# Kernel optimization log

Measured on AMD Instinct MI355X. Metric: run time of the kernel, lower is better.

Reference implementation:

```python
import jax, jax.numpy as jnp
import numpy as np

N = 65536        # total nodes
E = 2097152      # total edges (avg degree 32)
B = 1024         # graphs / proteins
FXD = 78         # atom feature dim
DIM = 32         # GIN hidden dim
EMB = 128        # protein embedding dim
OUTD = 128       # output_dim
VOCAB = 26       # CHARPROTLEN + 1
PLEN = 1000      # protein sequence length (conv in_channels)
KS = 8           # conv kernel size
CLEN = EMB - KS + 1  # 121
NF = 32          # n_filters


def setup_inputs() -> dict:
    key = jax.random.key(0)
    ks = jax.random.split(key, 30)
    g = lambda k, s: (jax.random.normal(k, s, dtype=jnp.float32) * 0.05)
    inp = {
        "x": jax.random.normal(ks[0], (N, FXD), dtype=jnp.float32),
        "edge_index": jax.random.randint(ks[1], (2, E), 0, N, dtype=jnp.int32),
        "batch": jnp.sort(jax.random.randint(ks[2], (N,), 0, B, dtype=jnp.int32)),
        "target": jax.random.randint(ks[3], (B, PLEN), 0, VOCAB, dtype=jnp.int32),
        # GIN layer 1 MLP
        "w1a": g(ks[4], (FXD, DIM)), "b1a": jnp.zeros((DIM,), jnp.float32),
        "w1b": g(ks[5], (DIM, DIM)), "b1b": jnp.zeros((DIM,), jnp.float32),
        # GIN layers 2-5 MLPs (stacked)
        "wa": g(ks[6], (4, DIM, DIM)), "ba": jnp.zeros((4, DIM), jnp.float32),
        "wb": g(ks[7], (4, DIM, DIM)), "bb": jnp.zeros((4, DIM), jnp.float32),
        # BatchNorm affine params for bn1..bn5
        "gamma": jnp.ones((5, DIM), jnp.float32),
        "beta": jnp.zeros((5, DIM), jnp.float32),
        # drug head
        "w_fcxd": g(ks[8], (DIM, OUTD)), "b_fcxd": jnp.zeros((OUTD,), jnp.float32),
        # protein branch
        "emb": g(ks[9], (VOCAB, EMB)),
        "conv_w": g(ks[10], (NF, PLEN, KS)),  # OIH layout
        "conv_b": jnp.zeros((NF,), jnp.float32),
        "w_fcxt": g(ks[11], (NF * CLEN, OUTD)), "b_fcxt": jnp.zeros((OUTD,), jnp.float32),
        # joint head
        "w_fc1": g(ks[12], (256, 1024)), "b_fc1": jnp.zeros((1024,), jnp.float32),
        "w_fc2": g(ks[13], (1024, 256)), "b_fc2": jnp.zeros((256,), jnp.float32),
        "w_out": g(ks[14], (256, 1)), "b_out": jnp.zeros((1,), jnp.float32),
    }
    return inp


def reference(x, edge_index, batch, target,
              w1a, b1a, w1b, b1b, wa, ba, wb, bb, gamma, beta,
              w_fcxd, b_fcxd, emb, conv_w, conv_b, w_fcxt, b_fcxt,
              w_fc1, b_fc1, w_fc2, b_fc2, w_out, b_out):
    n_nodes = x.shape[0]
    n_graphs = target.shape[0]
    src, dst = edge_index[0], edge_index[1]

    def gin_bn(h, wi, bi, wo, bo, g, bt):
        # GINConv (eps=0): nn((1+eps)*x + sum_{j->i} x_j), then ReLU, then BatchNorm1d (batch stats)
        agg = jax.ops.segment_sum(h[src], dst, num_segments=n_nodes) + h
        h = jnp.maximum(agg @ wi + bi, 0.0) @ wo + bo
        h = jnp.maximum(h, 0.0)
        m = h.mean(axis=0)
        v = h.var(axis=0)  # biased, matches torch BN normalization
        return g * (h - m) * jax.lax.rsqrt(v + 1e-5) + bt

    h = gin_bn(x, w1a, b1a, w1b, b1b, gamma[0], beta[0])
    for i in range(4):
        h = gin_bn(h, wa[i], ba[i], wb[i], bb[i], gamma[i + 1], beta[i + 1])

    # global add pool over graphs
    hg = jax.ops.segment_sum(h, batch, num_segments=n_graphs)  # [B, 32]
    xd = jnp.maximum(hg @ w_fcxd + b_fcxd, 0.0)  # [B, 128] (dropout inactive in eval)

    # protein branch: embed then Conv1d over the embedding axis (in_channels = seq positions)
    e = emb[target]  # [B, 1000, 128]
    c = jax.lax.conv_general_dilated(e, conv_w, window_strides=(1,), padding="VALID",
                                     dimension_numbers=("NCH", "OIH", "NCH"))
    c = c + conv_b[None, :, None]  # [B, 32, 121]
    xt = c.reshape(n_graphs, NF * CLEN) @ w_fcxt + b_fcxt  # [B, 128], no activation in original

    xc = jnp.concatenate([xd, xt], axis=1)  # [B, 256]
    xc = jnp.maximum(xc @ w_fc1 + b_fc1, 0.0)
    xc = jnp.maximum(xc @ w_fc2 + b_fc2, 0.0)
    return xc @ w_out + b_out  # [B, 1]
```

## Files before the change

### kernel.cpp

```cpp
#include <hip/hip_runtime.h>
#include <hip/hip_fp16.h>

#define N_NODES 65536
#define N_EDGES 2097152
#define NB      1024
#define FXD     78
#define DIM     32
#define EMBD    128
#define OUTD    128
#define VOCAB   26
#define PLEN    1000
#define KS      8
#define CLEN    121
#define NF      32
#define FCX     (NF*CLEN)
#define NBKT    256
#define EPB     8192
#define NSLICE  256
#define EROW2   156
#define ECHUNK  13


__global__ __launch_bounds__(256) void k_bhist(
    const int* __restrict__ ei, int* __restrict__ bktCnt)
{
    __shared__ int h[NBKT];
    int tid = threadIdx.x;
    h[tid] = 0;
    __syncthreads();
    long base = (long)blockIdx.x * EPB;
    #pragma unroll 4
    for (int q=0; q<EPB/256; ++q) {
        int d = ei[N_EDGES + base + q*256 + tid];
        atomicAdd(&h[d>>8], 1);
    }
    __syncthreads();
    atomicAdd(&bktCnt[tid], h[tid]);
}

__global__ __launch_bounds__(256) void k_bscan(
    const int* __restrict__ bktCnt, int* __restrict__ bktBase, int* __restrict__ bktCur)
{
    __shared__ int s[NBKT];
    int t = threadIdx.x;
    int v = bktCnt[t];
    s[t] = v;
    __syncthreads();
    for (int off=1; off<256; off<<=1) {
        int tv = (t >= off) ? s[t-off] : 0;
        __syncthreads();
        s[t] += tv;
        __syncthreads();
    }
    int ex = s[t] - v;
    bktBase[t] = ex;
    bktCur[t] = ex;
    if (t == 255) bktBase[256] = s[255];
}

__global__ __launch_bounds__(256) void k_bucketA(
    const int* __restrict__ ei, int* __restrict__ bktCur, unsigned int* __restrict__ pairs)
{
    __shared__ unsigned int raw[EPB];
    __shared__ unsigned int srt[EPB];
    __shared__ unsigned char bOf[EPB];
    __shared__ int hist[NBKT], sc[NBKT], lcur[NBKT], gbase[NBKT];
    int tid = threadIdx.x;
    hist[tid] = 0;
    __syncthreads();
    int eb = blockIdx.x * EPB;
    for (int i=tid; i<EPB; i+=256) {
        int s = ei[eb+i];
        int d = ei[N_EDGES+eb+i];
        raw[i] = ((unsigned int)d<<16) | (unsigned int)s;
        atomicAdd(&hist[d>>8], 1);
    }
    __syncthreads();
    int v = hist[tid];
    sc[tid] = v;
    __syncthreads();
    for (int off=1; off<256; off<<=1) {
        int tv = (tid >= off) ? sc[tid-off] : 0;
        __syncthreads();
        sc[tid] += tv;
        __syncthreads();
    }
    int ex = sc[tid] - v;
    sc[tid] = ex;
    lcur[tid] = ex;
    gbase[tid] = atomicAdd(&bktCur[tid], v);
    __syncthreads();
    for (int i=tid; i<EPB; i+=256) {
        unsigned int p = raw[i];
        int k = p >> 24;
        int pos = atomicAdd(&lcur[k], 1);
        srt[pos] = p;
        bOf[pos] = (unsigned char)k;
    }
    __syncthreads();
    for (int i=tid; i<EPB; i+=256) {
        int k = bOf[i];
        pairs[gbase[k] + (i - sc[k])] = srt[i];
    }
}

__global__ __launch_bounds__(256) void k_fillB(
    const int* __restrict__ bktBase, const unsigned int* __restrict__ pairs,
    int* __restrict__ rowptr, int* __restrict__ csr)
{
    __shared__ int hist[256], sc[256], cur[256];
    int b = blockIdx.x, tid = threadIdx.x;
    int node0 = b*256;
    hist[tid] = 0;
    __syncthreads();
    int s = bktBase[b], e = bktBase[b+1];
    for (int i = s + tid; i < e; i += 256)
        atomicAdd(&hist[(pairs[i] >> 16) & 255], 1);
    __syncthreads();
    int v = hist[tid];
    sc[tid] = v;
    __syncthreads();
    for (int off=1; off<256; off<<=1) {
        int tv = (tid >= off) ? sc[tid-off] : 0;
        __syncthreads();
        sc[tid] += tv;
        __syncthreads();
    }
    int base = s + sc[tid] - v;
    rowptr[node0 + tid] = base;
    cur[tid] = base;
    if (b == NBKT-1 && tid == 255) rowptr[N_NODES] = N_EDGES;
    __syncthreads();
    for (int i = s + tid; i < e; i += 256) {
        unsigned int p = pairs[i];
        int pos = atomicAdd(&cur[(p >> 16) & 255], 1);
        csr[pos] = (int)(p & 0xFFFFu);
    }
}


__global__ __launch_bounds__(256) void k_l1_transform(
    const float* __restrict__ x, const float* __restrict__ w,
    __half* __restrict__ t)
{
    __shared__ float wS[FXD*DIM];
    for (int i = threadIdx.x; i < FXD*DIM; i += 256) wS[i] = w[i];
    __syncthreads();
    int node = blockIdx.x*256 + threadIdx.x;
    float acc[DIM];
    #pragma unroll
    for (int d=0; d<DIM; ++d) acc[d] = 0.f;
    const float* xr = x + (long)node*FXD;
    for (int j=0; j<FXD; ++j) {
        float xv = xr[j];
        #pragma unroll
        for (int d=0; d<DIM; ++d) acc[d] += xv * wS[j*DIM+d];
    }
    union { __half2 h2[16]; uint4 u4[4]; } pk;
    #pragma unroll
    for (int q=0; q<16; ++q) pk.h2[q] = __floats2half2_rn(acc[2*q], acc[2*q+1]);
    uint4* dst4 = (uint4*)(t + (long)node*DIM);
    #pragma unroll
    for (int q=0; q<4; ++q) dst4[q] = pk.u4[q];
}

__global__ __launch_bounds__(256) void k_transform(
    const float* __restrict__ z, const float* __restrict__ part,
    const float* __restrict__ gamma, const float* __restrict__ beta, int layer,
    const float* __restrict__ w, __half* __restrict__ t)
{
    __shared__ float wS[DIM*DIM];
    __shared__ float red[4][64];
    __shared__ float sS[2*DIM];
    int tid = threadIdx.x;
    for (int i=tid; i<DIM*DIM; i+=256) wS[i] = w[i];
    {
        int ch = tid & 63, qq = tid >> 6;
        float s = 0.f;
        for (int i = qq*64; i < qq*64 + 64; ++i) s += part[(i<<6) + ch];
        red[qq][ch] = s;
    }
    __syncthreads();
    if (tid < DIM) {
        float tots = red[0][tid]+red[1][tid]+red[2][tid]+red[3][tid];
        float totq = red[0][DIM+tid]+red[1][DIM+tid]+red[2][DIM+tid]+red[3][DIM+tid];
        float mean = tots * (1.f/N_NODES);
        float var  = totq * (1.f/N_NODES) - mean*mean;
        float sc = gamma[layer*DIM+tid] * rsqrtf(var + 1e-5f);
        sS[tid] = sc;
        sS[DIM+tid] = beta[layer*DIM+tid] - mean*sc;
    }
    __syncthreads();
    int node = blockIdx.x*256 + tid;
    float h[DIM];
    const float4* z4 = (const float4*)(z + (long)node*DIM);
    #pragma unroll
    for (int q=0; q<DIM/4; ++q) {
        float4 v = z4[q];
        h[q*4+0]=v.x; h[q*4+1]=v.y; h[q*4+2]=v.z; h[q*4+3]=v.w;
    }
    #pragma unroll
    for (int d=0; d<DIM; ++d) h[d] = h[d]*sS[d] + sS[DIM+d];
    float acc[DIM];
    #pragma unroll
    for (int d=0; d<DIM; ++d) acc[d] = 0.f;
    #pragma unroll
    for (int j=0; j<DIM; ++j) {
        float hv = h[j];
        #pragma unroll
        for (int d=0; d<DIM; ++d) acc[d] += hv * wS[j*DIM+d];
    }
    union { __half2 h2[16]; uint4 u4[4]; } pk;
    #pragma unroll
    for (int q=0; q<16; ++q) pk.h2[q] = __floats2half2_rn(acc[2*q], acc[2*q+1]);
    uint4* dst4 = (uint4*)(t + (long)node*DIM);
    #pragma unroll
    for (int q=0; q<4; ++q) dst4[q] = pk.u4[q];
}

__global__ __launch_bounds__(256) void k_gather_mlp(
    const int* __restrict__ rowptr, const int* __restrict__ csr,
    const __half* __restrict__ t,
    const float* __restrict__ bi, const float* __restrict__ wo, const float* __restrict__ bo,
    float* __restrict__ z, float* __restrict__ part)
{
    __shared__ float wS[DIM*DIM];
    __shared__ float bS[2*DIM];
    __shared__ float stS[2*DIM];
    int tid = threadIdx.x;
    for (int i=tid; i<DIM*DIM; i+=256) wS[i]=wo[i];
    if (tid<DIM) bS[tid]=bi[tid];
    else if (tid<2*DIM) bS[tid]=bo[tid-DIM];
    if (tid<2*DIM) stS[tid]=0.f;
    __syncthreads();
    int g = tid >> 3;
    int l = tid & 7;
    int node = blockIdx.x*32 + g;
    const uint2* t4 = (const uint2*)t;
    uint2 sv = t4[(long)node*8 + l];
    float2 p0 = __half22float2(*(const __half2*)&sv.x);
    float2 p1 = __half22float2(*(const __half2*)&sv.y);
    float a0=p0.x, a1=p0.y, a2=p1.x, a3=p1.y;
    float c0=0.f, c1=0.f, c2=0.f, c3=0.f;
    int s0 = rowptr[node], s1 = rowptr[node+1];
    int e = s0;
    for (; e+8 <= s1; e+=8) {
        int myIdx = csr[e + l];
        #pragma unroll
        for (int k=0; k<8; ++k) {
            int idx = __shfl(myIdx, k, 8);
            uint2 v = t4[(long)idx*8 + l];
            float2 q0 = __half22float2(*(const __half2*)&v.x);
            float2 q1 = __half22float2(*(const __half2*)&v.y);
            if (k & 1) { c0+=q0.x; c1+=q0.y; c2+=q1.x; c3+=q1.y; }
            else       { a0+=q0.x; a1+=q0.y; a2+=q1.x; a3+=q1.y; }
        }
    }
    if (e+4 <= s1) {
        int myIdx = csr[e + (l & 3)];
        #pragma unroll
        for (int k=0; k<4; ++k) {
            int idx = __shfl(myIdx, k, 8);
            uint2 v = t4[(long)idx*8 + l];
            float2 q0 = __half22float2(*(const __half2*)&v.x);
            float2 q1 = __half22float2(*(const __half2*)&v.y);
            if (k & 1) { c0+=q0.x; c1+=q0.y; c2+=q1.x; c3+=q1.y; }
            else       { a0+=q0.x; a1+=q0.y; a2+=q1.x; a3+=q1.y; }
        }
        e += 4;
    }
    for (; e<s1; ++e) {
        uint2 v = t4[(long)csr[e]*8 + l];
        float2 q0 = __half22float2(*(const __half2*)&v.x);
        float2 q1 = __half22float2(*(const __half2*)&v.y);
        a0+=q0.x; a1+=q0.y; a2+=q1.x; a3+=q1.y;
    }
    float ua[4];
    ua[0] = fmaxf(a0+c0 + bS[4*l+0], 0.f);
    ua[1] = fmaxf(a1+c1 + bS[4*l+1], 0.f);
    ua[2] = fmaxf(a2+c2 + bS[4*l+2], 0.f);
    ua[3] = fmaxf(a3+c3 + bS[4*l+3], 0.f);
    float zz[4];
    #pragma unroll
    for (int q=0; q<4; ++q) zz[q] = bS[DIM + 4*l + q];
    const float4* w4 = (const float4*)wS;
    #pragma unroll
    for (int j=0; j<DIM; ++j) {
        float uj = __shfl(ua[j & 3], j >> 2, 8);
        float4 wv = w4[j*8 + l];
        zz[0]+=uj*wv.x; zz[1]+=uj*wv.y; zz[2]+=uj*wv.z; zz[3]+=uj*wv.w;
    }
    #pragma unroll
    for (int q=0; q<4; ++q) zz[q] = fmaxf(zz[q], 0.f);
    ((float4*)z)[(long)node*8 + l] = make_float4(zz[0], zz[1], zz[2], zz[3]);
    float sr[4], qr[4];
    #pragma unroll
    for (int q=0; q<4; ++q) { sr[q] = zz[q]; qr[q] = zz[q]*zz[q]; }
    #pragma unroll
    for (int q=0; q<4; ++q) {
        sr[q] += __shfl_down(sr[q], 32, 64); qr[q] += __shfl_down(qr[q], 32, 64);
        sr[q] += __shfl_down(sr[q], 16, 64); qr[q] += __shfl_down(qr[q], 16, 64);
        sr[q] += __shfl_down(sr[q],  8, 64); qr[q] += __shfl_down(qr[q],  8, 64);
    }
    if ((tid & 63) < 8) {
        #pragma unroll
        for (int q=0; q<4; ++q) {
            atomicAdd(&stS[4*l+q],       sr[q]);
            atomicAdd(&stS[DIM+4*l+q],   qr[q]);
        }
    }
    __syncthreads();
    if (tid < 2*DIM)
        atomicAdd(&part[((blockIdx.x & (NSLICE-1))<<6) + tid], stS[tid]);
}

__global__ __launch_bounds__(256) void k_scaleshift(
    const float* __restrict__ part,
    const float* __restrict__ gamma, const float* __restrict__ beta,
    int layer, float* __restrict__ ss)
{
    __shared__ float red[4][64];
    __shared__ float totS[64];
    int t = threadIdx.x;
    int ch = t & 63, q = t >> 6;
    float s = 0.f;
    for (int i = q*64; i < q*64 + 64; ++i) s += part[(i<<6) + ch];
    red[q][ch] = s;
    __syncthreads();
    if (t < 64) totS[t] = red[0][t]+red[1][t]+red[2][t]+red[3][t];
    __syncthreads();
    if (t < DIM) {
        float mean = totS[t] * (1.f/N_NODES);
        float var  = totS[DIM+t] * (1.f/N_NODES) - mean*mean;
        float sc = gamma[layer*DIM+t] * rsqrtf(var + 1e-5f);
        ss[t] = sc;
        ss[DIM+t] = beta[layer*DIM+t] - mean*sc;
    }
}

__global__ __launch_bounds__(256) void k_pool(
    const float* __restrict__ z, const float* __restrict__ ss,
    const int* __restrict__ batch, float* __restrict__ hg)
{
    int tid = threadIdx.x;
    int node = blockIdx.x*32 + (tid>>3);
    int cq = tid & 7;
    float4 v = ((const float4*)z)[(long)node*8 + cq];
    float4 sc = ((const float4*)ss)[cq];
    float4 sh = ((const float4*)ss)[8 + cq];
    v.x = v.x*sc.x + sh.x; v.y = v.y*sc.y + sh.y;
    v.z = v.z*sc.z + sh.z; v.w = v.w*sc.w + sh.w;
    int b = batch[node];
    int b0 = __shfl(b, 0, 64);
    int b7 = __shfl(b, 63, 64);
    if (b0 == b7) {
        #pragma unroll
        for (int off=8; off<64; off<<=1) {
            v.x += __shfl_xor(v.x, off, 64);
            v.y += __shfl_xor(v.y, off, 64);
            v.z += __shfl_xor(v.z, off, 64);
            v.w += __shfl_xor(v.w, off, 64);
        }
        if ((tid & 63) < 8) {
            float* dst = hg + (long)b0*DIM + cq*4;
            atomicAdd(dst+0, v.x); atomicAdd(dst+1, v.y);
            atomicAdd(dst+2, v.z); atomicAdd(dst+3, v.w);
        }
    } else {
        float* dst = hg + (long)b*DIM + cq*4;
        atomicAdd(dst+0, v.x); atomicAdd(dst+1, v.y);
        atomicAdd(dst+2, v.z); atomicAdd(dst+3, v.w);
    }
}

__global__ __launch_bounds__(128) void k_xd(
    const float* __restrict__ hg, const float* __restrict__ w,
    const float* __restrict__ bias, float* __restrict__ xc)
{
    int b = blockIdx.x, n = threadIdx.x;
    __shared__ float hS[DIM];
    if (n < DIM) hS[n] = hg[b*DIM+n];
    __syncthreads();
    float acc = bias[n];
    #pragma unroll
    for (int r=0; r<DIM; ++r) acc += hS[r]*w[r*OUTD+n];
    xc[b*256 + n] = fmaxf(acc, 0.f);
}


__global__ __launch_bounds__(256) void k_cw_transpose(
    const float* __restrict__ cw, __half* __restrict__ cwT)
{
    int g = blockIdx.x*256 + threadIdx.x;
    int i = g >> 8;
    int j = g & 255;
    int o = j >> 3, k = j & 7;
    cwT[g] = __float2half(cw[o*(PLEN*KS) + i*KS + k]);
}

__global__ __launch_bounds__(256) void k_convA(
    const int* __restrict__ target, const __half* __restrict__ cwTh,
    __half* __restrict__ G)
{
    __shared__ int sortedS[PLEN];
    __shared__ int meta[3*VOCAB+2];
    int* cntS = meta;
    int* segS = meta + VOCAB;
    int* curS = meta + 2*VOCAB + 1;
    int bb = blockIdx.x, j = threadIdx.x;
    int b = bb >> 1, sub = bb & 1;
    if (j < VOCAB) cntS[j] = 0;
    __syncthreads();
    int tloc[4];
    #pragma unroll
    for (int q=0; q<4; ++q) {
        int i = j + q*256;
        if (i < PLEN) {
            tloc[q] = target[b*PLEN+i];
            atomicAdd(&cntS[tloc[q]], 1);
        } else tloc[q] = -1;
    }
    __syncthreads();
    if (j == 0) {
        int run = 0;
        for (int v=0; v<VOCAB; ++v) { segS[v]=run; run += cntS[v]; }
        segS[VOCAB] = run;
    }
    __syncthreads();
    if (j < VOCAB) curS[j] = segS[j];
    __syncthreads();
    #pragma unroll
    for (int q=0; q<4; ++q) {
        int i = j + q*256;
        if (i < PLEN) {
            int pos = atomicAdd(&curS[tloc[q]], 1);
            sortedS[pos] = i;
        }
    }
    __syncthreads();
    int w = j >> 6;
    int lane = j & 63;
    int half32 = lane >> 5;
    int c32 = lane & 31;
    const uint4* cw4 = (const uint4*)cwTh;
    __half2 hz = __float2half2_rn(0.f);
    int v0 = 13*sub, v1 = v0 + 13;
    int segbase = segS[v0];
    int tot = segS[v1] - segbase;
    for (int v=v0; v<v1; ++v) {
        int s = segS[v], e2 = segS[v+1];
        int wv = (tot > 0) ? ((s - segbase)*4)/tot : 0;
        if (wv > 3) wv = 3;
        if (wv != w) continue;
        float facc[8];
        #pragma unroll
        for (int q=0; q<8; ++q) facc[q] = 0.f;
        int p = s;
        for (; p+16 <= e2; p += 16) {
            __half2 h0=hz, h1=hz, h2=hz, h3=hz;
            #pragma unroll
            for (int u=0; u<8; ++u) {
                int i0 = sortedS[p+2*u], i1 = sortedS[p+2*u+1];
                int row = half32 ? i1 : i0;
                uint4 q4 = cw4[row*32 + c32];
                const __half2* hh = (const __half2*)&q4;
                h0 = __hadd2(h0, hh[0]); h1 = __hadd2(h1, hh[1]);
                h2 = __hadd2(h2, hh[2]); h3 = __hadd2(h3, hh[3]);
            }
            float2 f0=__half22float2(h0), f1=__half22float2(h1),
                   f2=__half22float2(h2), f3=__half22float2(h3);
            facc[0]+=f0.x; facc[1]+=f0.y; facc[2]+=f1.x; facc[3]+=f1.y;
            facc[4]+=f2.x; facc[5]+=f2.y; facc[6]+=f3.x; facc[7]+=f3.y;
        }
        for (; p+2 <= e2; p += 2) {
            int i0 = sortedS[p], i1 = sortedS[p+1];
            int row = half32 ? i1 : i0;
            uint4 q4 = cw4[row*32 + c32];
            const __half2* hh = (const __half2*)&q4;
            float2 f0=__half22float2(hh[0]), f1=__half22float2(hh[1]),
                   f2=__half22float2(hh[2]), f3=__half22float2(hh[3]);
            facc[0]+=f0.x; facc[1]+=f0.y; facc[2]+=f1.x; facc[3]+=f1.y;
            facc[4]+=f2.x; facc[5]+=f2.y; facc[6]+=f3.x; facc[7]+=f3.y;
        }
        if (p < e2 && half32 == 0) {
            uint4 q4 = cw4[sortedS[p]*32 + c32];
            const __half2* hh = (const __half2*)&q4;
            float2 f0=__half22float2(hh[0]), f1=__half22float2(hh[1]),
                   f2=__half22float2(hh[2]), f3=__half22float2(hh[3]);
            facc[0]+=f0.x; facc[1]+=f0.y; facc[2]+=f1.x; facc[3]+=f1.y;
            facc[4]+=f2.x; facc[5]+=f2.y; facc[6]+=f3.x; facc[7]+=f3.y;
        }
        #pragma unroll
        for (int q=0; q<8; ++q) facc[q] += __shfl_xor(facc[q], 32, 64);
        if (half32 == 0) {
            __half2 o0 = __floats2half2_rn(facc[0], facc[1]);
            __half2 o1 = __floats2half2_rn(facc[2], facc[3]);
            __half2 o2 = __floats2half2_rn(facc[4], facc[5]);
            __half2 o3 = __floats2half2_rn(facc[6], facc[7]);
            uint4 pk;
            pk.x = *(unsigned int*)&o0; pk.y = *(unsigned int*)&o1;
            pk.z = *(unsigned int*)&o2; pk.w = *(unsigned int*)&o3;
            ((uint4*)(G + ((long)b*VOCAB + v)*256))[c32] = pk;
        }
    }
}

__global__ __launch_bounds__(256) void k_convB(
    const float* __restrict__ emb, const __half* __restrict__ G,
    const float* __restrict__ conv_b, float* __restrict__ c)
{
    __shared__ __align__(16) char buf[21632];
    __shared__ float cbS[NF];
    __half* GsH = (__half*)buf;
    float*  U   = (float*)(buf + 13312);
    float*  stage = (float*)buf;
    int b = blockIdx.x, j = threadIdx.x;
    if (j < NF) cbS[j] = conv_b[j];
    {
        const uint4* gsrc = (const uint4*)(G + (long)b*VOCAB*256);
        uint4* gdst = (uint4*)GsH;
        for (int i=j; i<832; i+=256) gdst[i] = gsrc[i];
    }
    int o = j >> 3, pg = j & 7;
    int t0 = pg*16;
    int tcnt = (t0+16 <= CLEN) ? 16 : (CLEN - t0);
    float out[16];
    __syncthreads();
    #pragma unroll
    for (int q=0; q<16; ++q) out[q] = cbS[o];
    for (int ch=0; ch<2; ++ch) {
        __syncthreads();
        for (int i=j; i<ECHUNK*EMBD; i+=256) {
            int v = i >> 7, tt = i & 127;
            U[v*EROW2 + tt + 4*(tt>>4)] = emb[(ch*ECHUNK + v)*EMBD + tt];
        }
        __syncthreads();
        for (int vv=0; vv<ECHUNK; ++vv) {
            uint4 gv = *(const uint4*)(GsH + (ch*ECHUNK+vv)*256 + o*8);
            const __half2* gh = (const __half2*)&gv;
            float2 ga = __half22float2(gh[0]), gb = __half22float2(gh[1]);
            float2 gc = __half22float2(gh[2]), gd = __half22float2(gh[3]);
            float g[8] = {ga.x,ga.y,gb.x,gb.y,gc.x,gc.y,gd.x,gd.y};
            const float* ev = &U[vv*EROW2 + 20*pg];
            float4 E0 = *(const float4*)(ev);
            float4 E1 = *(const float4*)(ev+4);
            float4 E2 = *(const float4*)(ev+8);
            float4 E3 = *(const float4*)(ev+12);
            float4 E4 = *(const float4*)(ev+20);
            float4 E5 = *(const float4*)(ev+24);
            float e[24] = {E0.x,E0.y,E0.z,E0.w, E1.x,E1.y,E1.z,E1.w,
                           E2.x,E2.y,E2.z,E2.w, E3.x,E3.y,E3.z,E3.w,
                           E4.x,E4.y,E4.z,E4.w, E5.x,E5.y,E5.z,E5.w};
            #pragma unroll
            for (int q=0; q<16; ++q) {
                float s = 0.f;
                #pragma unroll
                for (int k=0; k<KS; ++k) s += e[q+k]*g[k];
                out[q] += s;
            }
        }
    }
    __syncthreads();
    for (int q=0; q<tcnt; ++q) stage[o*CLEN + t0 + q] = out[q];
    __syncthreads();
    for (int idx=j; idx<FCX; idx+=256)
        c[(long)b*FCX + idx] = stage[idx];
}

#define XT_GB  16
#define XT_NS  16
#define XT_KS  (FCX/XT_NS)
#define XT_BK  22
#define XT_NCH (XT_KS/XT_BK)
__global__ __launch_bounds__(256) void k_xt(
    const float* __restrict__ c, const float* __restrict__ w,
    float* __restrict__ xtp)
{
    __shared__ float cS[XT_GB][XT_BK];
    __shared__ float wS[XT_BK][128];
    int b0 = blockIdx.x * XT_GB;
    int ks0 = blockIdx.y * XT_KS;
    int tid = threadIdx.x;
    int g2 = tid >> 5;
    int co = tid & 31;
    int cg0 = tid / XT_BK, ck0 = tid - cg0*XT_BK;
    int i1 = tid + 256;
    int cg1 = i1 / XT_BK, ck1 = i1 - cg1*XT_BK;
    float wreg[11], creg0, creg1;
    {
        int k0 = ks0;
        #pragma unroll
        for (int q=0; q<11; ++q) {
            int idx = tid + q*256;
            wreg[q] = w[(long)(k0 + (idx>>7))*OUTD + (idx & 127)];
        }
        creg0 = c[(long)(b0+cg0)*FCX + k0 + ck0];
        if (tid < 96) creg1 = c[(long)(b0+cg1)*FCX + k0 + ck1];
    }
    float acc[2][4];
    #pragma unroll
    for (int q=0; q<2; ++q)
      #pragma unroll
      for (int p=0; p<4; ++p) acc[q][p] = 0.f;
    for (int ch=0; ch<XT_NCH; ++ch) {
        #pragma unroll
        for (int q=0; q<11; ++q) {
            int idx = tid + q*256;
            wS[idx>>7][idx & 127] = wreg[q];
        }
        cS[cg0][ck0] = creg0;
        if (tid < 96) cS[cg1][ck1] = creg1;
        __syncthreads();
        if (ch+1 < XT_NCH) {
            int k0 = ks0 + (ch+1)*XT_BK;
            #pragma unroll
            for (int q=0; q<11; ++q) {
                int idx = tid + q*256;
                wreg[q] = w[(long)(k0 + (idx>>7))*OUTD + (idx & 127)];
            }
            creg0 = c[(long)(b0+cg0)*FCX + k0 + ck0];
            if (tid < 96) creg1 = c[(long)(b0+cg1)*FCX + k0 + ck1];
        }
        #pragma unroll
        for (int k2=0; k2<XT_BK/2; ++k2) {
            float2 cv0 = *(const float2*)&cS[2*g2  ][2*k2];
            float2 cv1 = *(const float2*)&cS[2*g2+1][2*k2];
            float4 wv0 = *(const float4*)&wS[2*k2  ][co*4];
            float4 wv1 = *(const float4*)&wS[2*k2+1][co*4];
            acc[0][0]+=cv0.x*wv0.x; acc[0][1]+=cv0.x*wv0.y;
            acc[0][2]+=cv0.x*wv0.z; acc[0][3]+=cv0.x*wv0.w;
            acc[1][0]+=cv1.x*wv0.x; acc[1][1]+=cv1.x*wv0.y;
            acc[1][2]+=cv1.x*wv0.z; acc[1][3]+=cv1.x*wv0.w;
            acc[0][0]+=cv0.y*wv1.x; acc[0][1]+=cv0.y*wv1.y;
            acc[0][2]+=cv0.y*wv1.z; acc[0][3]+=cv0.y*wv1.w;
            acc[1][0]+=cv1.y*wv1.x; acc[1][1]+=cv1.y*wv1.y;
            acc[1][2]+=cv1.y*wv1.z; acc[1][3]+=cv1.y*wv1.w;
        }
        __syncthreads();
    }
    #pragma unroll
    for (int q=0; q<2; ++q) {
        int g = b0 + 2*g2 + q;
        float4* dst = (float4*)(xtp + ((long)blockIdx.y*NB + g)*128);
        dst[co] = make_float4(acc[q][0], acc[q][1], acc[q][2], acc[q][3]);
    }
}

__global__ __launch_bounds__(256) void k_xt_red(
    const float* __restrict__ xtp, const float* __restrict__ bias,
    float* __restrict__ xc)
{
    int p = blockIdx.x*256 + threadIdx.x;
    int g = p >> 5, c4 = p & 31;
    const float4* src = (const float4*)xtp;
    float4 s = src[(long)g*32 + c4];
    #pragma unroll
    for (int y=1; y<XT_NS; ++y) {
        float4 v = src[((long)y*NB + g)*32 + c4];
        s.x += v.x; s.y += v.y; s.z += v.z; s.w += v.w;
    }
    float4 bv = ((const float4*)bias)[c4];
    s.x += bv.x; s.y += bv.y; s.z += bv.z; s.w += bv.w;
    ((float4*)(xc + g*256 + 128))[c4] = s;
}


#define FC1_NS 4
#define FC1_KR 64
__global__ __launch_bounds__(256) void k_fc1(
    const float* __restrict__ xc, const float* __restrict__ w,
    float* __restrict__ y1p)
{
    __shared__ float xS[4][FC1_KR];
    int b0 = blockIdx.x*4;
    int r0 = blockIdx.y*FC1_KR;
    int n = threadIdx.x;
    xS[n>>6][n&63] = xc[(b0 + (n>>6))*256 + r0 + (n&63)];
    __syncthreads();
    float acc[4][4];
    #pragma unroll
    for (int q=0;q<4;++q)
      #pragma unroll
      for (int m=0;m<4;++m) acc[q][m]=0.f;
    for (int r=0; r<FC1_KR; ++r) {
        float x0=xS[0][r], x1=xS[1][r], x2=xS[2][r], x3=xS[3][r];
        #pragma unroll
        for (int m=0; m<4; ++m) {
            float wv = w[(long)(r0+r)*1024 + m*256 + n];
            acc[0][m]+=x0*wv; acc[1][m]+=x1*wv;
            acc[2][m]+=x2*wv; acc[3][m]+=x3*wv;
        }
    }
    long base = ((long)blockIdx.y*NB + b0)*1024;
    #pragma unroll
    for (int q=0; q<4; ++q)
        #pragma unroll
        for (int m=0; m<4; ++m)
            y1p[base + (long)q*1024 + m*256 + n] = acc[q][m];
}

__global__ __launch_bounds__(256) void k_fc1_red(
    const float* __restrict__ y1p, const float* __restrict__ bias,
    float* __restrict__ y)
{
    int p = blockIdx.x*256 + threadIdx.x;
    int g = p >> 8, c4 = p & 255;
    const float4* src = (const float4*)y1p;
    float4 s = src[(long)g*256 + c4];
    #pragma unroll
    for (int yq=1; yq<FC1_NS; ++yq) {
        float4 v = src[((long)yq*NB + g)*256 + c4];
        s.x+=v.x; s.y+=v.y; s.z+=v.z; s.w+=v.w;
    }
    float4 bv = ((const float4*)bias)[c4];
    s.x = fmaxf(s.x+bv.x, 0.f); s.y = fmaxf(s.y+bv.y, 0.f);
    s.z = fmaxf(s.z+bv.z, 0.f); s.w = fmaxf(s.w+bv.w, 0.f);
    ((float4*)y)[(long)g*256 + c4] = s;
}

#define FC2_NS 8
#define FC2_KR 128
__global__ __launch_bounds__(256) void k_fc2(
    const float* __restrict__ y, const float* __restrict__ w,
    float* __restrict__ y2p)
{
    __shared__ float xS[4][FC2_KR];
    int b0 = blockIdx.x*4;
    int r0 = blockIdx.y*FC2_KR;
    int n = threadIdx.x;
    {
        int e1 = n + 256;
        xS[n>>7][n&127]   = y[(b0 + (n>>7))*1024  + r0 + (n&127)];
        xS[e1>>7][e1&127] = y[(b0 + (e1>>7))*1024 + r0 + (e1&127)];
    }
    __syncthreads();
    float acc[4] = {0.f, 0.f, 0.f, 0.f};
    for (int r=0; r<FC2_KR; ++r) {
        float wv = w[(long)(r0+r)*256 + n];
        acc[0]+=xS[0][r]*wv; acc[1]+=xS[1][r]*wv;
        acc[2]+=xS[2][r]*wv; acc[3]+=xS[3][r]*wv;
    }
    long base = ((long)blockIdx.y*NB + b0)*256;
    #pragma unroll
    for (int q=0; q<4; ++q) y2p[base + q*256 + n] = acc[q];
}

__global__ __launch_bounds__(256) void k_fc2_red(
    const float* __restrict__ y2p, const float* __restrict__ bias,
    float* __restrict__ y2)
{
    int p = blockIdx.x*256 + threadIdx.x;
    int g = p >> 6, c4 = p & 63;
    const float4* src = (const float4*)y2p;
    float4 s = src[(long)g*64 + c4];
    #pragma unroll
    for (int yq=1; yq<FC2_NS; ++yq) {
        float4 v = src[((long)yq*NB + g)*64 + c4];
        s.x+=v.x; s.y+=v.y; s.z+=v.z; s.w+=v.w;
    }
    float4 bv = ((const float4*)bias)[c4];
    s.x = fmaxf(s.x+bv.x, 0.f); s.y = fmaxf(s.y+bv.y, 0.f);
    s.z = fmaxf(s.z+bv.z, 0.f); s.w = fmaxf(s.w+bv.w, 0.f);
    ((float4*)y2)[(long)g*64 + c4] = s;
}

__global__ __launch_bounds__(256) void k_out(
    const float* __restrict__ y2, const float* __restrict__ w,
    const float* __restrict__ bias, float* __restrict__ out)
{
    int b = blockIdx.x, n = threadIdx.x;
    float v = y2[b*256 + n] * w[n];
    #pragma unroll
    for (int off=32; off; off>>=1) v += __shfl_down(v, off, 64);
    __shared__ float red[4];
    if ((n & 63) == 0) red[n >> 6] = v;
    __syncthreads();
    if (n == 0) out[b] = red[0]+red[1]+red[2]+red[3] + bias[0];
}


extern "C" void kernel_launch(void* const* d_in, const int* in_sizes, int n_in,
                              void* d_out, int out_size, void* d_ws, size_t ws_size,
                              hipStream_t stream) {
    const float* x      = (const float*)d_in[0];
    const int*   ei     = (const int*)  d_in[1];
    const int*   batch  = (const int*)  d_in[2];
    const int*   target = (const int*)  d_in[3];
    const float* w1a    = (const float*)d_in[4];
    const float* b1a    = (const float*)d_in[5];
    const float* w1b    = (const float*)d_in[6];
    const float* b1b    = (const float*)d_in[7];
    const float* wa     = (const float*)d_in[8];
    const float* ba     = (const float*)d_in[9];
    const float* wb     = (const float*)d_in[10];
    const float* bb     = (const float*)d_in[11];
    const float* gamma  = (const float*)d_in[12];
    const float* beta   = (const float*)d_in[13];
    const float* w_fcxd = (const float*)d_in[14];
    const float* b_fcxd = (const float*)d_in[15];
    const float* emb    = (const float*)d_in[16];
    const float* conv_w = (const float*)d_in[17];
    const float* conv_b = (const float*)d_in[18];
    const float* w_fcxt = (const float*)d_in[19];
    const float* b_fcxt = (const float*)d_in[20];
    const float* w_fc1  = (const float*)d_in[21];
    const float* b_fc1  = (const float*)d_in[22];
    const float* w_fc2  = (const float*)d_in[23];
    const float* b_fc2  = (const float*)d_in[24];
    const float* w_out  = (const float*)d_in[25];
    const float* b_out  = (const float*)d_in[26];

    float* ws      = (float*)d_ws;
    __half* tH     = (__half*)ws;
    float* z       = ws + 1048576;
    unsigned int* pairs = (unsigned int*)(z + (size_t)N_NODES*DIM);
    int*   csr     = (int*)(pairs + N_EDGES);
    int*   rowptr  = csr + N_EDGES;
    int*   bktCnt  = rowptr + (N_NODES + 8);
    int*   bktBase = bktCnt + 256;
    int*   bktCur  = bktBase + 264;
    float* ss      = (float*)(bktCur + 256);
    float* hg      = ss + 64;
    float* cwT     = hg + (size_t)NB*DIM;
    float* cbuf    = cwT + 256000;
    float* xc      = cbuf + (size_t)NB*FCX;
    float* y1      = xc + (size_t)NB*256;
    float* y2      = y1 + (size_t)NB*1024;
    float* part    = y2 + (size_t)NB*256;
    __half* cwTh   = (__half*)cwT;
    float* xtp     = z;
    __half* Gbuf   = (__half*)z;
    float* y1p     = ws;
    float* y2p     = ws + 4194304;

    hipMemsetAsync(bktCnt, 0, 256*sizeof(int), stream);
    k_bhist<<<NBKT, 256, 0, stream>>>(ei, bktCnt);
    k_bscan<<<1, 256, 0, stream>>>(bktCnt, bktBase, bktCur);
    k_bucketA<<<NBKT, 256, 0, stream>>>(ei, bktCur, pairs);
    k_fillB<<<NBKT, 256, 0, stream>>>(bktBase, pairs, rowptr, csr);

    k_cw_transpose<<<1000, 256, 0, stream>>>(conv_w, cwTh);
    k_convA<<<2*NB, 256, 0, stream>>>(target, cwTh, Gbuf);
    k_convB<<<NB, 256, 0, stream>>>(emb, Gbuf, conv_b, cbuf);
    k_xt<<<dim3(NB/XT_GB, XT_NS), 256, 0, stream>>>(cbuf, w_fcxt, xtp);
    k_xt_red<<<(NB*DIM)/256, 256, 0, stream>>>(xtp, b_fcxt, xc);

    hipMemsetAsync(part, 0, 5*NSLICE*64*sizeof(float), stream);
    for (int l=0; l<5; ++l) {
        if (l == 0)
            k_l1_transform<<<N_NODES/256, 256, 0, stream>>>(x, w1a, tH);
        else
            k_transform<<<N_NODES/256, 256, 0, stream>>>(
                z, part + (size_t)(l-1)*NSLICE*64, gamma, beta, l-1,
                wa + (size_t)(l-1)*DIM*DIM, tH);
        const float* bi = (l==0) ? b1a : ba + (size_t)(l-1)*DIM;
        const float* wo = (l==0) ? w1b : wb + (size_t)(l-1)*DIM*DIM;
        const float* bo = (l==0) ? b1b : bb + (size_t)(l-1)*DIM;
        k_gather_mlp<<<N_NODES/32, 256, 0, stream>>>(
            rowptr, csr, tH, bi, wo, bo, z, part + (size_t)l*NSLICE*64);
    }
    k_scaleshift<<<1, 256, 0, stream>>>(part + (size_t)4*NSLICE*64, gamma, beta, 4, ss);

    hipMemsetAsync(hg, 0, (size_t)NB*DIM*sizeof(float), stream);
    k_pool<<<N_NODES/32, 256, 0, stream>>>(z, ss, batch, hg);
    k_xd<<<NB, 128, 0, stream>>>(hg, w_fcxd, b_fcxd, xc);

    k_fc1<<<dim3(NB/4, FC1_NS), 256, 0, stream>>>(xc, w_fc1, y1p);
    k_fc1_red<<<1024, 256, 0, stream>>>(y1p, b_fc1, y1);
    k_fc2<<<dim3(NB/4, FC2_NS), 256, 0, stream>>>(y1, w_fc2, y2p);
    k_fc2_red<<<256, 256, 0, stream>>>(y2p, b_fc2, y2);
    k_out<<<NB, 256, 0, stream>>>(y2, w_out, b_out, (float*)d_out);
}
```

Measured before the change: 634.1 us.

## Fold embedding conv into fcxt weights and replace convB+xt with one GEMM

Precomputes a matrix combining the embedding table with the fcxt weights per vocab/filter/tap, plus a constant term for the conv bias. The protein projection then becomes a single GEMM of the per-graph histogram-like G tensor against that matrix, removing the convB kernel and the intermediate conv output. This trades a larger K dimension and fp16 G operands for skipping a kernel and its global round trip.

```diff
diff --git a/kernel.cpp b/kernel.cpp
--- a/kernel.cpp
+++ b/kernel.cpp
@@ -17,8 +17,6 @@
 #define NBKT    256
 #define EPB     8192
 #define NSLICE  256
-#define EROW2   156
-#define ECHUNK  13
 
 
 __global__ __launch_bounds__(256) void k_bhist(
@@ -505,136 +503,92 @@
     }
 }
 
-__global__ __launch_bounds__(256) void k_convB(
-    const float* __restrict__ emb, const __half* __restrict__ G,
-    const float* __restrict__ conv_b, float* __restrict__ c)
-{
-    __shared__ __align__(16) char buf[21632];
-    __shared__ float cbS[NF];
-    __half* GsH = (__half*)buf;
-    float*  U   = (float*)(buf + 13312);
-    float*  stage = (float*)buf;
-    int b = blockIdx.x, j = threadIdx.x;
-    if (j < NF) cbS[j] = conv_b[j];
-    {
-        const uint4* gsrc = (const uint4*)(G + (long)b*VOCAB*256);
-        uint4* gdst = (uint4*)GsH;
-        for (int i=j; i<832; i+=256) gdst[i] = gsrc[i];
-    }
-    int o = j >> 3, pg = j & 7;
-    int t0 = pg*16;
-    int tcnt = (t0+16 <= CLEN) ? 16 : (CLEN - t0);
-    float out[16];
-    __syncthreads();
-    #pragma unroll
-    for (int q=0; q<16; ++q) out[q] = cbS[o];
-    for (int ch=0; ch<2; ++ch) {
-        __syncthreads();
-        for (int i=j; i<ECHUNK*EMBD; i+=256) {
-            int v = i >> 7, tt = i & 127;
-            U[v*EROW2 + tt + 4*(tt>>4)] = emb[(ch*ECHUNK + v)*EMBD + tt];
-        }
-        __syncthreads();
-        for (int vv=0; vv<ECHUNK; ++vv) {
-            uint4 gv = *(const uint4*)(GsH + (ch*ECHUNK+vv)*256 + o*8);
-            const __half2* gh = (const __half2*)&gv;
-            float2 ga = __half22float2(gh[0]), gb = __half22float2(gh[1]);
-            float2 gc = __half22float2(gh[2]), gd = __half22float2(gh[3]);
-            float g[8] = {ga.x,ga.y,gb.x,gb.y,gc.x,gc.y,gd.x,gd.y};
-            const float* ev = &U[vv*EROW2 + 20*pg];
-            float4 E0 = *(const float4*)(ev);
-            float4 E1 = *(const float4*)(ev+4);
-            float4 E2 = *(const float4*)(ev+8);
-            float4 E3 = *(const float4*)(ev+12);
-            float4 E4 = *(const float4*)(ev+20);
-            float4 E5 = *(const float4*)(ev+24);
-            float e[24] = {E0.x,E0.y,E0.z,E0.w, E1.x,E1.y,E1.z,E1.w,
-                           E2.x,E2.y,E2.z,E2.w, E3.x,E3.y,E3.z,E3.w,
-                           E4.x,E4.y,E4.z,E4.w, E5.x,E5.y,E5.z,E5.w};
-            #pragma unroll
-            for (int q=0; q<16; ++q) {
-                float s = 0.f;
-                #pragma unroll
-                for (int k=0; k<KS; ++k) s += e[q+k]*g[k];
-                out[q] += s;
-            }
-        }
-    }
-    __syncthreads();
-    for (int q=0; q<tcnt; ++q) stage[o*CLEN + t0 + q] = out[q];
-    __syncthreads();
-    for (int idx=j; idx<FCX; idx+=256)
-        c[(long)b*FCX + idx] = stage[idx];
-}
-
-#define XT_GB  16
-#define XT_NS  16
-#define XT_KS  (FCX/XT_NS)
-#define XT_BK  22
-#define XT_NCH (XT_KS/XT_BK)
-__global__ __launch_bounds__(256) void k_xt(
-    const float* __restrict__ c, const float* __restrict__ w,
+__global__ __launch_bounds__(256) void k_mprep(
+    const float* __restrict__ emb, const float* __restrict__ w,
+    const float* __restrict__ conv_b, float* __restrict__ M,
+    float* __restrict__ C0)
+{
+    __shared__ float eS[EMBD];
+    int v = blockIdx.x >> 5, o = blockIdx.x & 31;
+    int tid = threadIdx.x;
+    if (tid < EMBD) eS[tid] = emb[v*EMBD + tid];
+    __syncthreads();
+    int n = tid & 127, kb = tid >> 7;
+    float acc[4] = {0.f, 0.f, 0.f, 0.f};
+    float c0 = 0.f;
+    const float* wp = w + (long)(o*CLEN)*OUTD + n;
+    for (int t2=0; t2<CLEN; ++t2) {
+        float wv = wp[(long)t2*OUTD];
+        c0 += wv;
+        #pragma unroll
+        for (int q=0; q<4; ++q) acc[q] += eS[t2 + kb + 2*q] * wv;
+    }
+    long base = ((long)(v*256 + o*8)) * 128 + n;
+    #pragma unroll
+    for (int q=0; q<4; ++q) M[base + (long)(kb + 2*q)*128] = acc[q];
+    if (v == 0 && kb == 0) atomicAdd(&C0[n], c0 * conv_b[o]);
+}
+
+#define XG_GB  16
+#define XG_NS  16
+#define XG_K   (VOCAB*256)
+#define XG_KS  (XG_K/XG_NS)
+#define XG_BK  32
+#define XG_NCH (XG_KS/XG_BK)
+__global__ __launch_bounds__(256) void k_xtg(
+    const __half* __restrict__ G, const float* __restrict__ M,
     float* __restrict__ xtp)
 {
-    __shared__ float cS[XT_GB][XT_BK];
-    __shared__ float wS[XT_BK][128];
-    int b0 = blockIdx.x * XT_GB;
-    int ks0 = blockIdx.y * XT_KS;
+    __shared__ float bS[XG_BK][128];
+    __shared__ __half aS[XG_GB][XG_BK];
+    int b0 = blockIdx.x * XG_GB;
+    int ks0 = blockIdx.y * XG_KS;
     int tid = threadIdx.x;
-    int g2 = tid >> 5;
-    int co = tid & 31;
-    int cg0 = tid / XT_BK, ck0 = tid - cg0*XT_BK;
-    int i1 = tid + 256;
-    int cg1 = i1 / XT_BK, ck1 = i1 - cg1*XT_BK;
-    float wreg[11], creg0, creg1;
+    int g2 = tid >> 5, co = tid & 31;
+    int ag = tid >> 4, au = tid & 15;
+    const unsigned int* G32 = (const unsigned int*)G;
+    float breg[16];
+    unsigned int areg;
     {
         int k0 = ks0;
         #pragma unroll
-        for (int q=0; q<11; ++q) {
+        for (int q=0; q<16; ++q) {
             int idx = tid + q*256;
-            wreg[q] = w[(long)(k0 + (idx>>7))*OUTD + (idx & 127)];
-        }
-        creg0 = c[(long)(b0+cg0)*FCX + k0 + ck0];
-        if (tid < 96) creg1 = c[(long)(b0+cg1)*FCX + k0 + ck1];
+            breg[q] = M[(long)(k0 + (idx>>7))*128 + (idx & 127)];
+        }
+        areg = G32[(long)(b0+ag)*3328 + (k0>>1) + au];
     }
     float acc[2][4];
     #pragma unroll
     for (int q=0; q<2; ++q)
       #pragma unroll
       for (int p=0; p<4; ++p) acc[q][p] = 0.f;
-    for (int ch=0; ch<XT_NCH; ++ch) {
-        #pragma unroll
-        for (int q=0; q<11; ++q) {
+    for (int ch=0; ch<XG_NCH; ++ch) {
+        #pragma unroll
+        for (int q=0; q<16; ++q) {
             int idx = tid + q*256;
-            wS[idx>>7][idx & 127] = wreg[q];
-        }
-        cS[cg0][ck0] = creg0;
-        if (tid < 96) cS[cg1][ck1] = creg1;
+            bS[idx>>7][idx & 127] = breg[q];
+        }
+        ((unsigned int*)aS)[ag*16 + au] = areg;
         __syncthreads();
-        if (ch+1 < XT_NCH) {
-            int k0 = ks0 + (ch+1)*XT_BK;
+        if (ch+1 < XG_NCH) {
+            int k0 = ks0 + (ch+1)*XG_BK;
             #pragma unroll
-            for (int q=0; q<11; ++q) {
+            for (int q=0; q<16; ++q) {
                 int idx = tid + q*256;
-                wreg[q] = w[(long)(k0 + (idx>>7))*OUTD + (idx & 127)];
+                breg[q] = M[(long)(k0 + (idx>>7))*128 + (idx & 127)];
             }
-            creg0 = c[(long)(b0+cg0)*FCX + k0 + ck0];
-            if (tid < 96) creg1 = c[(long)(b0+cg1)*FCX + k0 + ck1];
-        }
-        #pragma unroll
-        for (int k2=0; k2<XT_BK/2; ++k2) {
-            float2 cv0 = *(const float2*)&cS[2*g2  ][2*k2];
-            float2 cv1 = *(const float2*)&cS[2*g2+1][2*k2];
-            float4 wv0 = *(const float4*)&wS[2*k2  ][co*4];
-            float4 wv1 = *(const float4*)&wS[2*k2+1][co*4];
-            acc[0][0]+=cv0.x*wv0.x; acc[0][1]+=cv0.x*wv0.y;
-            acc[0][2]+=cv0.x*wv0.z; acc[0][3]+=cv0.x*wv0.w;
-            acc[1][0]+=cv1.x*wv0.x; acc[1][1]+=cv1.x*wv0.y;
-            acc[1][2]+=cv1.x*wv0.z; acc[1][3]+=cv1.x*wv0.w;
-            acc[0][0]+=cv0.y*wv1.x; acc[0][1]+=cv0.y*wv1.y;
-            acc[0][2]+=cv0.y*wv1.z; acc[0][3]+=cv0.y*wv1.w;
-            acc[1][0]+=cv1.y*wv1.x; acc[1][1]+=cv1.y*wv1.y;
-            acc[1][2]+=cv1.y*wv1.z; acc[1][3]+=cv1.y*wv1.w;
+            areg = G32[(long)(b0+ag)*3328 + (k0>>1) + au];
+        }
+        #pragma unroll
+        for (int kk=0; kk<XG_BK; ++kk) {
+            float a0 = __half2float(aS[2*g2  ][kk]);
+            float a1 = __half2float(aS[2*g2+1][kk]);
+            float4 wv = *(const float4*)&bS[kk][co*4];
+            acc[0][0]+=a0*wv.x; acc[0][1]+=a0*wv.y;
+            acc[0][2]+=a0*wv.z; acc[0][3]+=a0*wv.w;
+            acc[1][0]+=a1*wv.x; acc[1][1]+=a1*wv.y;
+            acc[1][2]+=a1*wv.z; acc[1][3]+=a1*wv.w;
         }
         __syncthreads();
     }
@@ -646,21 +600,23 @@
     }
 }
 
-__global__ __launch_bounds__(256) void k_xt_red(
+__global__ __launch_bounds__(256) void k_xtg_red(
     const float* __restrict__ xtp, const float* __restrict__ bias,
-    float* __restrict__ xc)
+    const float* __restrict__ C0, float* __restrict__ xc)
 {
     int p = blockIdx.x*256 + threadIdx.x;
     int g = p >> 5, c4 = p & 31;
     const float4* src = (const float4*)xtp;
     float4 s = src[(long)g*32 + c4];
     #pragma unroll
-    for (int y=1; y<XT_NS; ++y) {
+    for (int y=1; y<XG_NS; ++y) {
         float4 v = src[((long)y*NB + g)*32 + c4];
         s.x += v.x; s.y += v.y; s.z += v.z; s.w += v.w;
     }
     float4 bv = ((const float4*)bias)[c4];
-    s.x += bv.x; s.y += bv.y; s.z += bv.z; s.w += bv.w;
+    float4 cv = ((const float4*)C0)[c4];
+    s.x += bv.x + cv.x; s.y += bv.y + cv.y;
+    s.z += bv.z + cv.z; s.w += bv.w + cv.w;
     ((float4*)(xc + g*256 + 128))[c4] = s;
 }
 
@@ -828,8 +784,10 @@
     float* y2      = y1 + (size_t)NB*1024;
     float* part    = y2 + (size_t)NB*256;
     __half* cwTh   = (__half*)cwT;
-    float* xtp     = z;
     __half* Gbuf   = (__half*)z;
+    float* Mbuf    = cbuf;
+    float* C0buf   = cbuf + 851968;
+    float* xtp     = cbuf + 860160;
     float* y1p     = ws;
     float* y2p     = ws + 4194304;
 
@@ -839,11 +797,12 @@
     k_bucketA<<<NBKT, 256, 0, stream>>>(ei, bktCur, pairs);
     k_fillB<<<NBKT, 256, 0, stream>>>(bktBase, pairs, rowptr, csr);
 
+    hipMemsetAsync(C0buf, 0, 128*sizeof(float), stream);
     k_cw_transpose<<<1000, 256, 0, stream>>>(conv_w, cwTh);
+    k_mprep<<<VOCAB*32, 256, 0, stream>>>(emb, w_fcxt, conv_b, Mbuf, C0buf);
     k_convA<<<2*NB, 256, 0, stream>>>(target, cwTh, Gbuf);
-    k_convB<<<NB, 256, 0, stream>>>(emb, Gbuf, conv_b, cbuf);
-    k_xt<<<dim3(NB/XT_GB, XT_NS), 256, 0, stream>>>(cbuf, w_fcxt, xtp);
-    k_xt_red<<<(NB*DIM)/256, 256, 0, stream>>>(xtp, b_fcxt, xc);
+    k_xtg<<<dim3(NB/XG_GB, XG_NS), 256, 0, stream>>>(Gbuf, Mbuf, xtp);
+    k_xtg_red<<<(NB*DIM)/256, 256, 0, stream>>>(xtp, b_fcxt, C0buf, xc);
 
     hipMemsetAsync(part, 0, 5*NSLICE*64*sizeof(float), stream);
     for (int l=0; l<5; ++l) {
```

After: 625.8 us, median of 3. About the same (-1.3%).
